# Optimization experiments

Hardware: AMD Instinct MI355X
Metric: run time of the kernel (lower is better)

The kernel has to match this reference:

```python
import jax, jax.numpy as jnp
import numpy as np

DIM = 64          # hidden dim (hardwired in source)
N_FEAT = 11       # QM9 node features
E_FEAT = 5        # QM9 edge features (4 bond one-hot + distance)
N_GRAPHS = 128
NODES_PER = 20    # complete graphs (Complete transform)
N_NODES = N_GRAPHS * NODES_PER
EDGES_PER = NODES_PER * (NODES_PER - 1)  # 380, self-loops removed
N_EDGES = N_GRAPHS * EDGES_PER


def setup_inputs() -> dict:
    key = jax.random.key(0)
    ks = jax.random.split(key, 26)

    # complete-graph edge_index per graph (no self loops), block-contiguous batching
    r = np.repeat(np.arange(NODES_PER), NODES_PER)
    c = np.tile(np.arange(NODES_PER), NODES_PER)
    m = r != c
    r, c = r[m], c[m]
    offs = (np.arange(N_GRAPHS) * NODES_PER)[:, None]
    src = (r[None, :] + offs).reshape(-1)
    dst = (c[None, :] + offs).reshape(-1)
    edge_index = jnp.asarray(np.stack([src, dst]), dtype=jnp.int32)
    batch = jnp.asarray(np.repeat(np.arange(N_GRAPHS), NODES_PER), dtype=jnp.int32)

    def g(k, shape, scale=0.1):
        return jax.random.normal(k, shape, jnp.float32) * scale

    return {
        'x': jax.random.normal(ks[0], (N_NODES, N_FEAT), jnp.float32),
        'edge_index': edge_index,
        'edge_attr': jax.random.uniform(ks[1], (N_EDGES, E_FEAT), jnp.float32),
        'batch': batch,
        'lin0_w': g(ks[2], (N_FEAT, DIM)), 'lin0_b': g(ks[3], (DIM,)),
        'nn1_w': g(ks[4], (E_FEAT, 128)), 'nn1_b': g(ks[5], (128,)),
        'nn2_w': g(ks[6], (128, DIM * DIM), 0.02), 'nn2_b': g(ks[7], (DIM * DIM,), 0.02),
        'root_w': g(ks[8], (DIM, DIM)), 'conv_b': g(ks[9], (DIM,)),
        'gru_w_ih': g(ks[10], (3 * DIM, DIM)), 'gru_w_hh': g(ks[11], (3 * DIM, DIM)),
        'gru_b_ih': g(ks[12], (3 * DIM,)), 'gru_b_hh': g(ks[13], (3 * DIM,)),
        'lstm_w_ih': g(ks[14], (4 * DIM, 2 * DIM)), 'lstm_w_hh': g(ks[15], (4 * DIM, DIM)),
        'lstm_b_ih': g(ks[16], (4 * DIM,)), 'lstm_b_hh': g(ks[17], (4 * DIM,)),
        'lin1_w': g(ks[18], (2 * DIM, DIM)), 'lin1_b': g(ks[19], (DIM,)),
        'lin2_w': g(ks[20], (DIM, 1)), 'lin2_b': g(ks[21], (1,)),
    }


def reference(x, edge_index, edge_attr, batch,
              lin0_w, lin0_b, nn1_w, nn1_b, nn2_w, nn2_b, root_w, conv_b,
              gru_w_ih, gru_w_hh, gru_b_ih, gru_b_hh,
              lstm_w_ih, lstm_w_hh, lstm_b_ih, lstm_b_hh,
              lin1_w, lin1_b, lin2_w, lin2_b):
    N = x.shape[0]
    B = N_GRAPHS
    src, dst = edge_index[0], edge_index[1]

    # edge MLP -> per-edge [DIM, DIM] transforms (computed once; edge_attr fixed)
    h1 = jax.nn.relu(edge_attr @ nn1_w + nn1_b)
    We = (h1 @ nn2_w + nn2_b).reshape(-1, DIM, DIM)   # [E, DIM, DIM]
    deg = jnp.maximum(
        jax.ops.segment_sum(jnp.ones_like(dst, jnp.float32), dst, N), 1.0)

    out = jax.nn.relu(x @ lin0_w + lin0_b)
    h = out
    for _ in range(3):
        # NNConv: gather - per-edge matvec - scatter-mean, plus root & bias
        msg = jnp.einsum('ei,eio->eo', out[src], We)
        agg = jax.ops.segment_sum(msg, dst, N) / deg[:, None]
        m = jax.nn.relu(agg + out @ root_w + conv_b)
        # GRU cell (torch gate order r, z, n)
        gi = m @ gru_w_ih.T + gru_b_ih
        gh = h @ gru_w_hh.T + gru_b_hh
        r = jax.nn.sigmoid(gi[:, :DIM] + gh[:, :DIM])
        z = jax.nn.sigmoid(gi[:, DIM:2 * DIM] + gh[:, DIM:2 * DIM])
        n = jnp.tanh(gi[:, 2 * DIM:] + r * gh[:, 2 * DIM:])
        h = (1.0 - z) * n + z * h
        out = h

    # Set2Set pooling, 3 processing steps (torch LSTM gate order i, f, g, o)
    q_star = jnp.zeros((B, 2 * DIM), x.dtype)
    hl = jnp.zeros((B, DIM), x.dtype)
    cl = jnp.zeros((B, DIM), x.dtype)
    for _ in range(3):
        gates = q_star @ lstm_w_ih.T + lstm_b_ih + hl @ lstm_w_hh.T + lstm_b_hh
        i_g, f_g, g_g, o_g = jnp.split(gates, 4, axis=1)
        cl = jax.nn.sigmoid(f_g) * cl + jax.nn.sigmoid(i_g) * jnp.tanh(g_g)
        hl = jax.nn.sigmoid(o_g) * jnp.tanh(cl)
        q = hl
        e = jnp.sum(out * q[batch], axis=-1)
        emax = jax.ops.segment_max(e, batch, B)
        ex = jnp.exp(e - emax[batch])
        esum = jax.ops.segment_sum(ex, batch, B)
        a = ex / esum[batch]
        rvec = jax.ops.segment_sum(a[:, None] * out, batch, B)
        q_star = jnp.concatenate([q, rvec], axis=1)

    y = jax.nn.relu(q_star @ lin1_w + lin1_b) @ lin2_w + lin2_b
    return y.reshape(-1)
```

## Files before the change

### kernel.cpp

```cpp
#include <hip/hip_runtime.h>
#include <hip/hip_fp16.h>

#define DIMH 64
#define NFEAT 11
#define EFEAT 5
#define NG   128
#define NPG  20
#define NNODES (NG*NPG)
#define EPG  (NPG*(NPG-1))
#define NEDGES (NG*EPG)
#define H1D  128
#define KTOT (H1D*DIMH)
#define DEGV 19.0f
#define NCH  16

typedef __attribute__((ext_vector_type(8))) _Float16 f16x8;
typedef __attribute__((ext_vector_type(4))) float    f32x4;

__global__ __launch_bounds__(256) void k_prep(
    const float* __restrict__ x, const float* __restrict__ lin0w,
    const float* __restrict__ lin0b,
    const float* __restrict__ ea, const float* __restrict__ nn1w,
    const float* __restrict__ nn1b,
    const float* __restrict__ nn2w, const float* __restrict__ nn2b,
    const float* __restrict__ rootw,
    const float* __restrict__ lwih, const float* __restrict__ lwhh,
    float* __restrict__ out, _Float16* __restrict__ h1c,
    _Float16* __restrict__ WT2, _Float16* __restrict__ WpT2,
    float* __restrict__ wab) {
  int b = blockIdx.x, t = threadIdx.x;
  if (b < 2048) {
    int idx = b * 256 + t;
    int j = idx & 7, l = (idx >> 3) & 63, nf = (idx >> 9) & 3;
    int ks = (idx >> 11) & 15, ko = idx >> 15;
    float v = nn2w[(size_t)(ko * 8 + j) * 4096 + (ks * 4 + (l >> 4)) * 64 +
                   nf * 16 + (l & 15)];
    WT2[idx] = (_Float16)(v * (1.f / DEGV));
  } else if (b < 2688) {
    int idx = (b - 2048) * 256 + t;
    int n = idx >> 6, o = idx & 63;
    float acc = lin0b[o];
#pragma unroll
    for (int j = 0; j < NFEAT; ++j) acc += x[n * NFEAT + j] * lin0w[j * DIMH + o];
    out[idx] = fmaxf(acc, 0.f);
  } else if (b < 2878) {
    int e = (b - 2688) * 256 + t;
    float ef[EFEAT];
#pragma unroll
    for (int f = 0; f < EFEAT; ++f) ef[f] = ea[e * EFEAT + f];
    for (int ko = 0; ko < 16; ++ko) {
      f16x8 hv;
#pragma unroll
      for (int j = 0; j < 8; ++j) {
        int k = ko * 8 + j;
        float acc = nn1b[k];
#pragma unroll
        for (int f = 0; f < EFEAT; ++f) acc += ef[f] * nn1w[f * H1D + k];
        hv[j] = (_Float16)fmaxf(acc, 0.f);
      }
      ((f16x8*)h1c)[(size_t)ko * NEDGES + e] = hv;
    }
  } else if (b < 2894) {
    int idx = (b - 2878) * 256 + t;
    int jp = idx & 7, l = (idx >> 3) & 63, nf = (idx >> 9) & 3;
    int ks = (idx >> 11) & 1;
    int o = nf * 16 + (l & 15);
    int j = ks * 32 + (l >> 4) * 8 + jp;
    WpT2[idx] = (_Float16)(rootw[j * 64 + o] - nn2b[j * 64 + o] * (1.f / DEGV));
  } else {
    int idx = (b - 2894) * 256 + t;
    int row = idx >> 7, col = idx & 127;
    float v = lwih[(size_t)row * 128 + col];
    if (col < 64) v += lwhh[(size_t)row * 64 + col];
    wab[idx] = v;
  }
}

__global__ __launch_bounds__(256, 4) void k_pg(const _Float16* __restrict__ h1c,
                                               const float* __restrict__ out,
                                               const _Float16* __restrict__ WT2,
                                               const _Float16* __restrict__ WpT2,
                                               const float* __restrict__ nn2b,
                                               const float* __restrict__ convb,
                                               float* __restrict__ bgc,
                                               _Float16* __restrict__ part) {
  int ko = blockIdx.x, g = blockIdx.y;
  int t = threadIdx.x;
  __shared__ alignas(16) f16x8 h1s[EPG];
  __shared__ alignas(16) _Float16 Ps[NPG][520];
  __shared__ float sgl[64];
  __shared__ alignas(16) _Float16 AoT[NPG][64];
  int i = t & 63, w = t >> 6;
  int la = i & 15, hi = i >> 4;
  int m = w & 1, nfb = (w >> 1) * 2;
  float xr[NPG];
  _Float16 xh[NPG];
#pragma unroll
  for (int r = 0; r < NPG; ++r) {
    xr[r] = out[((size_t)g * NPG + r) * 64 + i];
    xh[r] = (_Float16)xr[r];
  }
  if (ko == 0 && t < 64) {
    float s = 0.f;
#pragma unroll
    for (int r = 0; r < NPG; ++r) s += xr[r];
    sgl[t] = s;
  }
  {
    const f16x8* src = (const f16x8*)h1c + ((size_t)ko * NEDGES + (size_t)g * EPG);
    for (int el = t; el < EPG; el += 256) h1s[el] = src[el];
  }
  __syncthreads();
  if (ko == 0 && t < 64) {
    float acc = convb[t];
    for (int ii = 0; ii < 64; ++ii)
      acc += sgl[ii] * nn2b[ii * 64 + t] * (1.f / DEGV);
    bgc[g * 64 + t] = acc;
  }
  {
#pragma unroll
    for (int cc = 0; cc < 5; ++cc) {
      int c = w + cc * 4;
      f16x8 acc = {(_Float16)0.f, (_Float16)0.f, (_Float16)0.f, (_Float16)0.f,
                   (_Float16)0.f, (_Float16)0.f, (_Float16)0.f, (_Float16)0.f};
#pragma unroll
      for (int r = 0; r < NPG; ++r) {
        if (r == c) continue;
        int el = r * 19 + c - (c > r ? 1 : 0);
        acc += h1s[el] * xh[r];
      }
      *(f16x8*)&Ps[c][i * 8] = acc;
    }
  }
  __syncthreads();
  f32x4 acc0 = {0.f, 0.f, 0.f, 0.f}, acc1 = {0.f, 0.f, 0.f, 0.f};
  const f16x8* B = (const f16x8*)WT2;
  int arow = m ? 4 + la : la;
#pragma unroll
  for (int ks = 0; ks < 16; ++ks) {
    f16x8 a = *(const f16x8*)&Ps[arow][(ks * 4 + hi) * 8];
    f16x8 b0 = B[(size_t)(((ko * 16 + ks) * 4 + nfb) * 64 + i)];
    f16x8 b1 = B[(size_t)(((ko * 16 + ks) * 4 + nfb + 1) * 64 + i)];
    acc0 = __builtin_amdgcn_mfma_f32_16x16x32_f16(a, b0, acc0, 0, 0, 0);
    acc1 = __builtin_amdgcn_mfma_f32_16x16x32_f16(a, b1, acc1, 0, 0, 0);
  }
  if (ko == 15) {
    if (w == 0) {
#pragma unroll
      for (int r = 0; r < NPG; ++r) AoT[r][i] = xh[r];
    }
    __syncthreads();
    const f16x8* W2f = (const f16x8*)WpT2;
#pragma unroll
    for (int ks2 = 0; ks2 < 2; ++ks2) {
      f16x8 a = *(const f16x8*)&AoT[arow][ks2 * 32 + hi * 8];
      f16x8 b0 = W2f[(size_t)((ks2 * 4 + nfb) * 64 + i)];
      f16x8 b1 = W2f[(size_t)((ks2 * 4 + nfb + 1) * 64 + i)];
      acc0 = __builtin_amdgcn_mfma_f32_16x16x32_f16(a, b0, acc0, 0, 0, 0);
      acc1 = __builtin_amdgcn_mfma_f32_16x16x32_f16(a, b1, acc1, 0, 0, 0);
    }
  }
  if (m == 0) {
    if (hi == 0) {
#pragma unroll
      for (int q = 0; q < 4; ++q) {
        size_t base = ((size_t)(g * NPG + q) * NCH + ko) * 64;
        part[base + nfb * 16 + la] = (_Float16)acc0[q];
        part[base + (nfb + 1) * 16 + la] = (_Float16)acc1[q];
      }
    }
  } else {
#pragma unroll
    for (int q = 0; q < 4; ++q) {
      int row = 4 + hi * 4 + q;
      size_t base = ((size_t)(g * NPG + row) * NCH + ko) * 64;
      part[base + nfb * 16 + la] = (_Float16)acc0[q];
      part[base + (nfb + 1) * 16 + la] = (_Float16)acc1[q];
    }
  }
}

#define NLOC 10
__global__ __launch_bounds__(512, 1) void k_gru(
    const _Float16* __restrict__ part, const float* __restrict__ bgc,
    const float* __restrict__ wih, const float* __restrict__ whh,
    const float* __restrict__ bih, const float* __restrict__ bhh,
    float* __restrict__ out) {
  __shared__ float outs[NLOC][64];
  __shared__ float ms[NLOC][64];
  __shared__ float gi_s[NLOC][192];
  __shared__ float gh_s[NLOC][192];
  int t = threadIdx.x;
  int b = blockIdx.x, g = b >> 1, nbase = (b & 1) * NLOC;
  int role = (t < 192) ? 0 : ((t >= 256 && t < 448) ? 1 : -1);
  int r = (t < 192) ? t : t - 256;
  float4 wreg[16];
  if (role == 0) {
    const float4* src = (const float4*)(wih + (size_t)r * 64);
#pragma unroll
    for (int q = 0; q < 16; ++q) wreg[q] = src[q];
  } else if (role == 1) {
    const float4* src = (const float4*)(whh + (size_t)r * 64);
#pragma unroll
    for (int q = 0; q < 16; ++q) wreg[q] = src[q];
  }
  if (t < NLOC * 16)
    ((float4*)&outs[0][0])[t] =
        ((const float4*)(out + ((size_t)g * NPG + nbase) * 64))[t];
  __syncthreads();
  int o = t & 63, n0 = t >> 6;
  {
    float base = bgc[g * 64 + o];
#pragma unroll
    for (int k = 0; k < 2; ++k) {
      int n = n0 + k * 8;
      if (n < NLOC) {
        float a = base;
#pragma unroll
        for (int c = 0; c < NCH; ++c)
          a += (float)part[((size_t)(g * NPG + nbase + n) * NCH + c) * 64 + o];
        ms[n][o] = fmaxf(a, 0.f);
      }
    }
  }
  __syncthreads();
  if (role == 0) {
    for (int n = 0; n < NLOC; ++n) {
      float acc = 0.f;
#pragma unroll
      for (int q = 0; q < 16; ++q) {
        float4 xv = *(const float4*)&ms[n][q * 4];
        acc += wreg[q].x * xv.x + wreg[q].y * xv.y +
               wreg[q].z * xv.z + wreg[q].w * xv.w;
      }
      gi_s[n][r] = acc;
    }
  } else if (role == 1) {
    for (int n = 0; n < NLOC; ++n) {
      float acc = 0.f;
#pragma unroll
      for (int q = 0; q < 16; ++q) {
        float4 xv = *(const float4*)&outs[n][q * 4];
        acc += wreg[q].x * xv.x + wreg[q].y * xv.y +
               wreg[q].z * xv.z + wreg[q].w * xv.w;
      }
      gh_s[n][r] = acc;
    }
  }
  __syncthreads();
  {
    float bir = bih[o], biz = bih[64 + o], bin = bih[128 + o];
    float bhr = bhh[o], bhz = bhh[64 + o], bhn = bhh[128 + o];
#pragma unroll
    for (int k = 0; k < 2; ++k) {
      int n = n0 + k * 8;
      if (n < NLOC) {
        float rr = 1.f / (1.f + expf(-(gi_s[n][o] + bir + gh_s[n][o] + bhr)));
        float zz = 1.f / (1.f + expf(-(gi_s[n][64 + o] + biz +
                                       gh_s[n][64 + o] + bhz)));
        float nc = tanhf(gi_s[n][128 + o] + bin +
                         rr * (gh_s[n][128 + o] + bhn));
        out[((size_t)g * NPG + nbase + n) * DIMH + o] =
            (1.f - zz) * nc + zz * outs[n][o];
      }
    }
  }
}

__global__ __launch_bounds__(512, 1) void k_ms2s(
    const _Float16* __restrict__ part, const float* __restrict__ bgc,
    const float* __restrict__ wih, const float* __restrict__ whh,
    const float* __restrict__ bih, const float* __restrict__ bhh,
    const float* __restrict__ out,
    const float* __restrict__ wab,
    const float* __restrict__ lbih, const float* __restrict__ lbhh,
    const float* __restrict__ l1w, const float* __restrict__ l1b,
    const float* __restrict__ l2w, const float* __restrict__ l2b,
    float* __restrict__ y) {
  __shared__ float outs[NPG][64];
  __shared__ float ms[NPG][64];
  __shared__ float gi_s[NPG][192];
  __shared__ float gh_s[NPG][192];
  __shared__ float qstar[2 * DIMH];
  __shared__ float hls[DIMH];
  __shared__ float es_s[NPG];
  __shared__ float gates_s[4][DIMH];
  __shared__ float hnew[NPG][64];
  int t = threadIdx.x;
  int g = blockIdx.x;
  int role = (t < 192) ? 0 : ((t >= 256 && t < 448) ? 1 : -1);
  int r = (t < 192) ? t : t - 256;
  float4 wreg[16];
  if (role == 0) {
    const float4* src = (const float4*)(wih + (size_t)r * 64);
#pragma unroll
    for (int q = 0; q < 16; ++q) wreg[q] = src[q];
  } else if (role == 1) {
    const float4* src = (const float4*)(whh + (size_t)r * 64);
#pragma unroll
    for (int q = 0; q < 16; ++q) wreg[q] = src[q];
  }
  if (t < NPG * 16)
    ((float4*)&outs[0][0])[t] = ((const float4*)(out + (size_t)g * NPG * 64))[t];
  __syncthreads();
  int o = t & 63, n0 = t >> 6;
  {
    float base = bgc[g * 64 + o];
#pragma unroll
    for (int k = 0; k < 3; ++k) {
      int n = n0 + k * 8;
      if (n < NPG) {
        float a = base;
#pragma unroll
        for (int c = 0; c < NCH; ++c)
          a += (float)part[((size_t)(g * NPG + n) * NCH + c) * 64 + o];
        ms[n][o] = fmaxf(a, 0.f);
      }
    }
  }
  __syncthreads();
  if (role == 0) {
    for (int n = 0; n < NPG; ++n) {
      float acc = 0.f;
#pragma unroll
      for (int q = 0; q < 16; ++q) {
        float4 xv = *(const float4*)&ms[n][q * 4];
        acc += wreg[q].x * xv.x + wreg[q].y * xv.y +
               wreg[q].z * xv.z + wreg[q].w * xv.w;
      }
      gi_s[n][r] = acc;
    }
  } else if (role == 1) {
    for (int n = 0; n < NPG; ++n) {
      float acc = 0.f;
#pragma unroll
      for (int q = 0; q < 16; ++q) {
        float4 xv = *(const float4*)&outs[n][q * 4];
        acc += wreg[q].x * xv.x + wreg[q].y * xv.y +
               wreg[q].z * xv.z + wreg[q].w * xv.w;
      }
      gh_s[n][r] = acc;
    }
  }
  __syncthreads();
  {
    float bir = bih[o], biz = bih[64 + o], bin = bih[128 + o];
    float bhr = bhh[o], bhz = bhh[64 + o], bhn = bhh[128 + o];
#pragma unroll
    for (int k = 0; k < 3; ++k) {
      int n = n0 + k * 8;
      if (n < NPG) {
        float rr = 1.f / (1.f + expf(-(gi_s[n][o] + bir + gh_s[n][o] + bhr)));
        float zz = 1.f / (1.f + expf(-(gi_s[n][64 + o] + biz +
                                       gh_s[n][64 + o] + bhz)));
        float nc = tanhf(gi_s[n][128 + o] + bin +
                         rr * (gh_s[n][128 + o] + bhn));
        hnew[n][o] = (1.f - zz) * nc + zz * outs[n][o];
      }
    }
  }
  if (t < 128) qstar[t] = 0.f;
  if (t < 64) hls[t] = 0.f;
  float cl = 0.f;
  __syncthreads();
  int q = t >> 6;
  const float4* wa = (const float4*)(wab + (size_t)(q * 64 + o) * 128);
  float bsum = (t < 256) ? (lbih[q * 64 + o] + lbhh[q * 64 + o]) : 0.f;
  for (int step = 0; step < 3; ++step) {
    if (t < 256) {
      float acc = bsum;
      if (step > 0) {
#pragma unroll
        for (int j4 = 0; j4 < 16; ++j4) {
          float4 w = wa[j4];
          float4 xv = *(const float4*)&hls[j4 * 4];
          acc += w.x * xv.x + w.y * xv.y + w.z * xv.z + w.w * xv.w;
        }
#pragma unroll
        for (int j4 = 0; j4 < 16; ++j4) {
          float4 w = wa[16 + j4];
          float4 xv = *(const float4*)&qstar[DIMH + j4 * 4];
          acc += w.x * xv.x + w.y * xv.y + w.z * xv.z + w.w * xv.w;
        }
      }
      gates_s[q][o] = acc;
    }
    __syncthreads();
    if (t < 64) {
      float gi = gates_s[0][t], gf = gates_s[1][t];
      float gg = gates_s[2][t], go = gates_s[3][t];
      cl = 1.f / (1.f + expf(-gf)) * cl + 1.f / (1.f + expf(-gi)) * tanhf(gg);
      float hv = 1.f / (1.f + expf(-go)) * tanhf(cl);
      hls[t] = hv; qstar[t] = hv;
    }
    __syncthreads();
    if (t < NPG) {
      float e = 0.f;
#pragma unroll
      for (int j4 = 0; j4 < 16; ++j4) {
        float4 a = *(const float4*)&hnew[t][j4 * 4];
        float4 b = *(const float4*)&hls[j4 * 4];
        e += a.x * b.x + a.y * b.y + a.z * b.z + a.w * b.w;
      }
      es_s[t] = e;
    }
    __syncthreads();
    if (t < 64) {
      float mx = -1e30f;
#pragma unroll
      for (int rr = 0; rr < NPG; ++rr) mx = fmaxf(mx, es_s[rr]);
      float sm = 0.f, rv = 0.f;
#pragma unroll
      for (int rr = 0; rr < NPG; ++rr) {
        float ex = expf(es_s[rr] - mx);
        sm += ex;
        rv += ex * hnew[rr][t];
      }
      qstar[DIMH + t] = rv / sm;
    }
    __syncthreads();
  }
  if (t < 64) {
    float acc = l1b[t];
    for (int j = 0; j < 2 * DIMH; ++j) acc += qstar[j] * l1w[j * DIMH + t];
    float v = fmaxf(acc, 0.f) * l2w[t];
    for (int off = 32; off > 0; off >>= 1) v += __shfl_down(v, off);
    if (t == 0) y[g] = v + l2b[0];
  }
}

extern "C" void kernel_launch(void* const* d_in, const int* in_sizes, int n_in,
                              void* d_out, int out_size, void* d_ws, size_t ws_size,
                              hipStream_t stream) {
  const float* x     = (const float*)d_in[0];
  const float* ea    = (const float*)d_in[2];
  const float* lin0w = (const float*)d_in[4];
  const float* lin0b = (const float*)d_in[5];
  const float* nn1w  = (const float*)d_in[6];
  const float* nn1b  = (const float*)d_in[7];
  const float* nn2w  = (const float*)d_in[8];
  const float* nn2b  = (const float*)d_in[9];
  const float* rootw = (const float*)d_in[10];
  const float* convb = (const float*)d_in[11];
  const float* gwih  = (const float*)d_in[12];
  const float* gwhh  = (const float*)d_in[13];
  const float* gbih  = (const float*)d_in[14];
  const float* gbhh  = (const float*)d_in[15];
  const float* lwih  = (const float*)d_in[16];
  const float* lwhh  = (const float*)d_in[17];
  const float* lbih  = (const float*)d_in[18];
  const float* lbhh  = (const float*)d_in[19];
  const float* l1w   = (const float*)d_in[20];
  const float* l1b   = (const float*)d_in[21];
  const float* l2w   = (const float*)d_in[22];
  const float* l2b   = (const float*)d_in[23];
  float* yout = (float*)d_out;

  char* ws = (char*)d_ws;
  float*    out  = (float*)ws;
  _Float16* h1c  = (_Float16*)(ws + 655360);
  _Float16* WT2  = (_Float16*)(ws + 13107200);
  _Float16* WpT2 = (_Float16*)(ws + 14155776);
  float*    bgc  = (float*)(ws + 14163968);
  _Float16* part = (_Float16*)(ws + 14196736);
  float*    wab  = (float*)(ws + 19439616);
  (void)ws_size; (void)in_sizes; (void)n_in; (void)out_size;

  k_prep<<<3022, 256, 0, stream>>>(x, lin0w, lin0b, ea, nn1w, nn1b,
                                   nn2w, nn2b, rootw, lwih, lwhh,
                                   out, h1c, WT2, WpT2, wab);
  for (int it = 0; it < 2; ++it) {
    k_pg<<<dim3(NCH, NG), 256, 0, stream>>>(h1c, out, WT2, WpT2, nn2b, convb,
                                            bgc, part);
    k_gru<<<NG * 2, 512, 0, stream>>>(part, bgc, gwih, gwhh, gbih, gbhh, out);
  }
  k_pg<<<dim3(NCH, NG), 256, 0, stream>>>(h1c, out, WT2, WpT2, nn2b, convb,
                                          bgc, part);
  k_ms2s<<<NG, 512, 0, stream>>>(part, bgc, gwih, gwhh, gbih, gbhh, out,
                                 wab, lbih, lbhh,
                                 l1w, l1b, l2w, l2b, yout);
}
```

Before: 136.2 us.

## Unfuse final GRU from Set2Set kernel and coalesce nn2 weight reads in prep

```diff
diff --git a/kernel.cpp b/kernel.cpp
--- a/kernel.cpp
+++ b/kernel.cpp
@@ -31,11 +31,14 @@
   int b = blockIdx.x, t = threadIdx.x;
   if (b < 2048) {
     int idx = b * 256 + t;
-    int j = idx & 7, l = (idx >> 3) & 63, nf = (idx >> 9) & 3;
-    int ks = (idx >> 11) & 15, ko = idx >> 15;
-    float v = nn2w[(size_t)(ko * 8 + j) * 4096 + (ks * 4 + (l >> 4)) * 64 +
-                   nf * 16 + (l & 15)];
-    WT2[idx] = (_Float16)(v * (1.f / DEGV));
+    int k128 = idx >> 12, rest = idx & 4095;
+    int i = rest >> 6, o = rest & 63;
+    int ko = k128 >> 3, j = k128 & 7;
+    int ks = i >> 2;
+    int l = (i & 3) * 16 + (o & 15);
+    int nf = o >> 4;
+    size_t dst = ((size_t)((ko * 16 + ks) * 4 + nf) * 64 + l) * 8 + j;
+    WT2[dst] = (_Float16)(nn2w[idx] * (1.f / DEGV));
   } else if (b < 2688) {
     int idx = (b - 2048) * 256 + t;
     int n = idx >> 6, o = idx & 63;
@@ -267,107 +270,30 @@
   }
 }
 
-__global__ __launch_bounds__(512, 1) void k_ms2s(
-    const _Float16* __restrict__ part, const float* __restrict__ bgc,
-    const float* __restrict__ wih, const float* __restrict__ whh,
-    const float* __restrict__ bih, const float* __restrict__ bhh,
-    const float* __restrict__ out,
+__global__ __launch_bounds__(256) void k_s2s(
+    const float* __restrict__ hn,
     const float* __restrict__ wab,
     const float* __restrict__ lbih, const float* __restrict__ lbhh,
     const float* __restrict__ l1w, const float* __restrict__ l1b,
     const float* __restrict__ l2w, const float* __restrict__ l2b,
     float* __restrict__ y) {
-  __shared__ float outs[NPG][64];
-  __shared__ float ms[NPG][64];
-  __shared__ float gi_s[NPG][192];
-  __shared__ float gh_s[NPG][192];
+  int g = blockIdx.x, t = threadIdx.x;
+  __shared__ float hs[NPG][DIMH];
   __shared__ float qstar[2 * DIMH];
   __shared__ float hls[DIMH];
   __shared__ float es_s[NPG];
   __shared__ float gates_s[4][DIMH];
-  __shared__ float hnew[NPG][64];
-  int t = threadIdx.x;
-  int g = blockIdx.x;
-  int role = (t < 192) ? 0 : ((t >= 256 && t < 448) ? 1 : -1);
-  int r = (t < 192) ? t : t - 256;
-  float4 wreg[16];
-  if (role == 0) {
-    const float4* src = (const float4*)(wih + (size_t)r * 64);
-#pragma unroll
-    for (int q = 0; q < 16; ++q) wreg[q] = src[q];
-  } else if (role == 1) {
-    const float4* src = (const float4*)(whh + (size_t)r * 64);
-#pragma unroll
-    for (int q = 0; q < 16; ++q) wreg[q] = src[q];
-  }
-  if (t < NPG * 16)
-    ((float4*)&outs[0][0])[t] = ((const float4*)(out + (size_t)g * NPG * 64))[t];
-  __syncthreads();
-  int o = t & 63, n0 = t >> 6;
-  {
-    float base = bgc[g * 64 + o];
-#pragma unroll
-    for (int k = 0; k < 3; ++k) {
-      int n = n0 + k * 8;
-      if (n < NPG) {
-        float a = base;
-#pragma unroll
-        for (int c = 0; c < NCH; ++c)
-          a += (float)part[((size_t)(g * NPG + n) * NCH + c) * 64 + o];
-        ms[n][o] = fmaxf(a, 0.f);
-      }
-    }
-  }
-  __syncthreads();
-  if (role == 0) {
-    for (int n = 0; n < NPG; ++n) {
-      float acc = 0.f;
-#pragma unroll
-      for (int q = 0; q < 16; ++q) {
-        float4 xv = *(const float4*)&ms[n][q * 4];
-        acc += wreg[q].x * xv.x + wreg[q].y * xv.y +
-               wreg[q].z * xv.z + wreg[q].w * xv.w;
-      }
-      gi_s[n][r] = acc;
-    }
-  } else if (role == 1) {
-    for (int n = 0; n < NPG; ++n) {
-      float acc = 0.f;
-#pragma unroll
-      for (int q = 0; q < 16; ++q) {
-        float4 xv = *(const float4*)&outs[n][q * 4];
-        acc += wreg[q].x * xv.x + wreg[q].y * xv.y +
-               wreg[q].z * xv.z + wreg[q].w * xv.w;
-      }
-      gh_s[n][r] = acc;
-    }
-  }
-  __syncthreads();
-  {
-    float bir = bih[o], biz = bih[64 + o], bin = bih[128 + o];
-    float bhr = bhh[o], bhz = bhh[64 + o], bhn = bhh[128 + o];
-#pragma unroll
-    for (int k = 0; k < 3; ++k) {
-      int n = n0 + k * 8;
-      if (n < NPG) {
-        float rr = 1.f / (1.f + expf(-(gi_s[n][o] + bir + gh_s[n][o] + bhr)));
-        float zz = 1.f / (1.f + expf(-(gi_s[n][64 + o] + biz +
-                                       gh_s[n][64 + o] + bhz)));
-        float nc = tanhf(gi_s[n][128 + o] + bin +
-                         rr * (gh_s[n][128 + o] + bhn));
-        hnew[n][o] = (1.f - zz) * nc + zz * outs[n][o];
-      }
-    }
-  }
+  for (int idx = t; idx < NPG * 16; idx += 256)
+    ((float4*)&hs[0][0])[idx] = ((const float4*)(hn + (size_t)g * NPG * 64))[idx];
   if (t < 128) qstar[t] = 0.f;
   if (t < 64) hls[t] = 0.f;
   float cl = 0.f;
   __syncthreads();
-  int q = t >> 6;
+  int q = t >> 6, o = t & 63;
   const float4* wa = (const float4*)(wab + (size_t)(q * 64 + o) * 128);
-  float bsum = (t < 256) ? (lbih[q * 64 + o] + lbhh[q * 64 + o]) : 0.f;
+  float bsum = lbih[q * 64 + o] + lbhh[q * 64 + o];
   for (int step = 0; step < 3; ++step) {
-    if (t < 256) {
+    {
       float acc = bsum;
       if (step > 0) {
 #pragma unroll
@@ -398,7 +324,7 @@
       float e = 0.f;
 #pragma unroll
       for (int j4 = 0; j4 < 16; ++j4) {
-        float4 a = *(const float4*)&hnew[t][j4 * 4];
+        float4 a = *(const float4*)&hs[t][j4 * 4];
         float4 b = *(const float4*)&hls[j4 * 4];
         e += a.x * b.x + a.y * b.y + a.z * b.z + a.w * b.w;
       }
@@ -414,7 +340,7 @@
       for (int rr = 0; rr < NPG; ++rr) {
         float ex = expf(es_s[rr] - mx);
         sm += ex;
-        rv += ex * hnew[rr][t];
+        rv += ex * hs[rr][t];
       }
       qstar[DIMH + t] = rv / sm;
     }
@@ -469,14 +395,11 @@
   k_prep<<<3022, 256, 0, stream>>>(x, lin0w, lin0b, ea, nn1w, nn1b,
                                    nn2w, nn2b, rootw, lwih, lwhh,
                                    out, h1c, WT2, WpT2, wab);
-  for (int it = 0; it < 2; ++it) {
+  for (int it = 0; it < 3; ++it) {
     k_pg<<<dim3(NCH, NG), 256, 0, stream>>>(h1c, out, WT2, WpT2, nn2b, convb,
                                             bgc, part);
     k_gru<<<NG * 2, 512, 0, stream>>>(part, bgc, gwih, gwhh, gbih, gbhh, out);
   }
-  k_pg<<<dim3(NCH, NG), 256, 0, stream>>>(h1c, out, WT2, WpT2, nn2b, convb,
-                                          bgc, part);
-  k_ms2s<<<NG, 512, 0, stream>>>(part, bgc, gwih, gwhh, gbih, gbhh, out,
-                                 wab, lbih, lbhh,
-                                 l1w, l1b, l2w, l2b, yout);
+  k_s2s<<<NG, 256, 0, stream>>>(out, wab, lbih, lbhh,
+                                l1w, l1b, l2w, l2b, yout);
 }
```

Measured after the change: 130.7 us. 1.04x faster.
